# Kernel optimization log

Hardware: AMD Instinct MI355X
Metric: run time of the kernel (lower is better)

## Reference

```python
import jax, jax.numpy as jnp
import numpy as np

N_NODES = 50000
N_EDGES = 800000
VOCAB = 100000
EMB = 64
HID = 64
N_CLASSES = 10
N_GRAPHS = 512


def setup_inputs() -> dict:
    key = jax.random.key(0)
    ks = jax.random.split(key, 12)
    node_ids = jax.random.randint(ks[0], (N_NODES,), 0, VOCAB)
    edge_index = jax.random.randint(ks[1], (2, N_EDGES), 0, N_NODES)
    batch = jnp.sort(jax.random.randint(ks[2], (N_NODES,), 0, N_GRAPHS))
    emb = jax.random.normal(ks[3], (VOCAB, EMB), jnp.float32)
    s_e = 1.0 / np.sqrt(EMB)
    s_h = 1.0 / np.sqrt(HID)
    Wl0 = jax.random.normal(ks[4], (EMB, HID), jnp.float32) * s_e
    bl0 = jnp.zeros((HID,), jnp.float32)
    Wr0 = jax.random.normal(ks[5], (EMB, HID), jnp.float32) * s_e
    Wl1 = jax.random.normal(ks[6], (HID, HID), jnp.float32) * s_h
    bl1 = jnp.zeros((HID,), jnp.float32)
    Wr1 = jax.random.normal(ks[7], (HID, HID), jnp.float32) * s_h
    Wout = jax.random.normal(ks[8], (HID, N_CLASSES), jnp.float32) * s_h
    bout = jnp.zeros((N_CLASSES,), jnp.float32)
    return {"node_ids": node_ids, "edge_index": edge_index, "batch": batch,
            "emb": emb, "Wl0": Wl0, "bl0": bl0, "Wr0": Wr0,
            "Wl1": Wl1, "bl1": bl1, "Wr1": Wr1, "Wout": Wout, "bout": bout}


def _sage_conv(x, src, dst, Wl, bl, Wr):
    # PyG SAGEConv (aggr='mean'): out_i = lin_l(mean_{j in N(i)} x_j) + lin_r(x_i)
    msg = x[src]                                      # [E, d] gather
    s = jax.ops.segment_sum(msg, dst, num_segments=N_NODES)
    cnt = jax.ops.segment_sum(jnp.ones((msg.shape[0], 1), x.dtype), dst,
                              num_segments=N_NODES)
    mean = jnp.where(cnt > 0, s / jnp.maximum(cnt, 1), 0)
    return mean @ Wl + bl + x @ Wr


def reference(node_ids, edge_index, batch, emb, Wl0, bl0, Wr0, Wl1, bl1, Wr1, Wout, bout):
    x = emb[node_ids]                                  # [N, EMB]
    src, dst = edge_index[0], edge_index[1]
    x = jax.nn.relu(_sage_conv(x, src, dst, Wl0, bl0, Wr0))
    x = jax.nn.relu(_sage_conv(x, src, dst, Wl1, bl1, Wr1))
    # global_mean_pool over graph ids
    s = jax.ops.segment_sum(x, batch, num_segments=N_GRAPHS)
    cnt = jax.ops.segment_sum(jnp.ones((x.shape[0], 1), x.dtype), batch,
                              num_segments=N_GRAPHS)
    pooled = jnp.where(cnt > 0, s / jnp.maximum(cnt, 1), 0)   # [G, HID]
    return pooled @ Wout + bout                        # [G, N_CLASSES]
```

## Files before the change

kernel.cpp:

```cpp
#include <hip/hip_runtime.h>
#include <hip/hip_bf16.h>

#define N_NODES 50000
#define N_EDGES 800000
#define EMB 64
#define HID 64
#define N_CLASSES 10
#define N_GRAPHS 512

#define BKT_SHIFT 6
#define BKT_NODES 64
#define NB_BKT ((N_NODES + BKT_NODES - 1) / BKT_NODES)
#define BKT_CAP 1408
#define CNT_STRIDE 16
#define EB_CHUNK 4096
#define EB_PER_THR (EB_CHUNK / 256)
#define EB_BLOCKS ((N_EDGES + EB_CHUNK - 1) / EB_CHUNK)
#define XFORM_BLOCKS ((N_NODES + 63) / 64)
#define XPAD 68
#define ZROW N_NODES
#define LCSR_SZ 1856
#define LCSR_FULL 1864

#define ACC8(vv, A)                                                            \
    do {                                                                       \
        A[0] += __uint_as_float((vv).x << 16);                                 \
        A[1] += __uint_as_float((vv).x & 0xFFFF0000u);                         \
        A[2] += __uint_as_float((vv).y << 16);                                 \
        A[3] += __uint_as_float((vv).y & 0xFFFF0000u);                         \
        A[4] += __uint_as_float((vv).z << 16);                                 \
        A[5] += __uint_as_float((vv).z & 0xFFFF0000u);                         \
        A[6] += __uint_as_float((vv).w << 16);                                 \
        A[7] += __uint_as_float((vv).w & 0xFFFF0000u);                         \
    } while (0)

__device__ __forceinline__ void build_local_csr(
    int bucket, const int* __restrict__ cnt, const int* __restrict__ ebuf,
    unsigned short* lcsr, int* nhist, int* sval, int* sexcl, int* ncur) {
    int tid = threadIdx.x;
    int bs = bucket * BKT_CAP;
    int ne = min(cnt[bucket * CNT_STRIDE], BKT_CAP);
    if (tid < BKT_NODES) { nhist[tid] = 0; ncur[tid] = 0; }
    for (int i = tid; i < LCSR_FULL; i += 256) lcsr[i] = (unsigned short)ZROW;
    __syncthreads();
    int held[6];
    int nh = 0;
    for (int i = tid; i < ne; i += 256) held[nh++] = ebuf[bs + i];
#pragma unroll
    for (int j = 0; j < 6; j++)
        if (j < nh) atomicAdd(&nhist[held[j] >> 16], 1);
    __syncthreads();
    if (tid < 64) {
        int v = nhist[tid];
        int p = (v + 7) & ~7;
        int s = p;
#pragma unroll
        for (int off = 1; off < 64; off <<= 1) {
            int u = __shfl_up(s, off, 64);
            if (tid >= off) s += u;
        }
        sval[tid] = v;
        sexcl[tid] = s - p;
    }
    __syncthreads();
#pragma unroll
    for (int j = 0; j < 6; j++)
        if (j < nh) {
            int p = held[j];
            int l = p >> 16;
            int r = atomicAdd(&ncur[l], 1);
            lcsr[sexcl[l] + r] = (unsigned short)(p & 0xFFFF);
        }
    __syncthreads();
}

__device__ __forceinline__ void agg2(
    int sA, int dA, int sB, int dB, int sl,
    const unsigned short* lcsr, const __hip_bfloat16* __restrict__ Pb,
    float oA[8], float oB[8]) {
    float a0[8], a1[8], b0[8], b1[8];
#pragma unroll
    for (int j = 0; j < 8; j++) { a0[j] = 0.f; a1[j] = 0.f; b0[j] = 0.f; b1[j] = 0.f; }
    int nA = (dA + 3) >> 2, nB = (dB + 3) >> 2;
    int n = max(nA, nB);
    int mA = max(nA - 1, 0), mB = max(nB - 1, 0);
    if (n > 0) {
        uint4 A0[4], A1[4], B0[4], B1[4];
#define LD4(D, base_)                                                          \
        {                                                                      \
            int _p = (base_);                                                  \
            D[0] = ((const uint4*)(Pb + (size_t)lcsr[_p + 0] * 64))[sl];       \
            D[1] = ((const uint4*)(Pb + (size_t)lcsr[_p + 1] * 64))[sl];       \
            D[2] = ((const uint4*)(Pb + (size_t)lcsr[_p + 2] * 64))[sl];       \
            D[3] = ((const uint4*)(Pb + (size_t)lcsr[_p + 3] * 64))[sl];       \
        }
#define AC4(S, X0, X1)                                                         \
        { ACC8(S[0], X0); ACC8(S[1], X1); ACC8(S[2], X0); ACC8(S[3], X1); }
        LD4(A0, sA); LD4(B0, sB);
        int c = 1;
        for (; c + 1 < n; c += 2) {
            LD4(A1, sA + 4 * min(c, mA)); LD4(B1, sB + 4 * min(c, mB));
            if (c - 1 < nA) AC4(A0, a0, a1);
            if (c - 1 < nB) AC4(B0, b0, b1);
            LD4(A0, sA + 4 * min(c + 1, mA)); LD4(B0, sB + 4 * min(c + 1, mB));
            if (c < nA) AC4(A1, a0, a1);
            if (c < nB) AC4(B1, b0, b1);
        }
        if (c < n) {
            LD4(A1, sA + 4 * min(c, mA)); LD4(B1, sB + 4 * min(c, mB));
            if (c - 1 < nA) AC4(A0, a0, a1);
            if (c - 1 < nB) AC4(B0, b0, b1);
            if (c < nA) AC4(A1, a0, a1);
            if (c < nB) AC4(B1, b0, b1);
        } else {
            if (c - 1 < nA) AC4(A0, a0, a1);
            if (c - 1 < nB) AC4(B0, b0, b1);
        }
#undef LD4
#undef AC4
    }
    float invA = (dA > 0) ? 1.0f / (float)dA : 0.0f;
    float invB = (dB > 0) ? 1.0f / (float)dB : 0.0f;
#pragma unroll
    for (int j = 0; j < 8; j++) {
        oA[j] = (a0[j] + a1[j]) * invA;
        oB[j] = (b0[j] + b1[j]) * invB;
    }
}

__device__ __forceinline__ void finish_row(int node, int sl,
                                           const float* __restrict__ H,
                                           float m[8], float* dst) {
    if (node < N_NODES) {
        size_t off = (size_t)node * 64 + sl * 8;
        float4 q0 = *(const float4*)&H[off];
        float4 q1 = *(const float4*)&H[off + 4];
        m[0] = fmaxf(m[0] + q0.x, 0.f);
        m[1] = fmaxf(m[1] + q0.y, 0.f);
        m[2] = fmaxf(m[2] + q0.z, 0.f);
        m[3] = fmaxf(m[3] + q0.w, 0.f);
        m[4] = fmaxf(m[4] + q1.x, 0.f);
        m[5] = fmaxf(m[5] + q1.y, 0.f);
        m[6] = fmaxf(m[6] + q1.z, 0.f);
        m[7] = fmaxf(m[7] + q1.w, 0.f);
    } else {
#pragma unroll
        for (int j = 0; j < 8; j++) m[j] = 0.f;
    }
    *(float4*)&dst[sl * 8] = make_float4(m[0], m[1], m[2], m[3]);
    *(float4*)&dst[sl * 8 + 4] = make_float4(m[4], m[5], m[6], m[7]);
}

__device__ __forceinline__ void gemm_dual_from_sX(
    int tile, int t, const float* sX,
    const float* __restrict__ Wl, const float* __restrict__ Wr,
    const float* __restrict__ bl,
    __hip_bfloat16* __restrict__ Pb, float* __restrict__ Qout) {
    int dg = t & 15, ng = t >> 4;
    float accL[4][4], accR[4][4];
#pragma unroll
    for (int i = 0; i < 4; i++)
#pragma unroll
        for (int j = 0; j < 4; j++) { accL[i][j] = 0.f; accR[i][j] = 0.f; }
#pragma unroll 4
    for (int k = 0; k < 64; k++) {
        float4 wl = ((const float4*)Wl)[k * 16 + dg];
        float4 wr = ((const float4*)Wr)[k * 16 + dg];
#pragma unroll
        for (int i = 0; i < 4; i++) {
            float xv = sX[(ng + i * 16) * XPAD + k];
            accL[i][0] = fmaf(xv, wl.x, accL[i][0]);
            accL[i][1] = fmaf(xv, wl.y, accL[i][1]);
            accL[i][2] = fmaf(xv, wl.z, accL[i][2]);
            accL[i][3] = fmaf(xv, wl.w, accL[i][3]);
            accR[i][0] = fmaf(xv, wr.x, accR[i][0]);
            accR[i][1] = fmaf(xv, wr.y, accR[i][1]);
            accR[i][2] = fmaf(xv, wr.z, accR[i][2]);
            accR[i][3] = fmaf(xv, wr.w, accR[i][3]);
        }
    }
    float4 blv = ((const float4*)bl)[dg];
#pragma unroll
    for (int i = 0; i < 4; i++) {
        int node = tile + ng + i * 16;
        if (node < N_NODES) {
            union { ushort4 u; __hip_bfloat16 h[4]; } pk;
            pk.h[0] = __float2bfloat16(accL[i][0]);
            pk.h[1] = __float2bfloat16(accL[i][1]);
            pk.h[2] = __float2bfloat16(accL[i][2]);
            pk.h[3] = __float2bfloat16(accL[i][3]);
            *(ushort4*)&Pb[(size_t)node * 64 + dg * 4] = pk.u;
            *(float4*)&Qout[(size_t)node * 64 + dg * 4] =
                make_float4(accR[i][0] + blv.x, accR[i][1] + blv.y,
                            accR[i][2] + blv.z, accR[i][3] + blv.w);
        }
    }
}

__global__ __launch_bounds__(256) void k_combo(
    const int* __restrict__ esrc, const int* __restrict__ edst,
    int* __restrict__ cnt, int* __restrict__ ebuf,
    const int* __restrict__ ids, const float* __restrict__ emb,
    const float* __restrict__ Wl, const float* __restrict__ bl,
    const float* __restrict__ Wr,
    __hip_bfloat16* __restrict__ Pb, __hip_bfloat16* __restrict__ Pb1z,
    float* __restrict__ Qout) {
    __shared__ float sX[64 * XPAD];
    int t = threadIdx.x;
    if (blockIdx.x < EB_BLOCKS) {
        if (blockIdx.x == 0 && t < 16) {
            uint4 z = make_uint4(0u, 0u, 0u, 0u);
            if (t < 8) ((uint4*)(Pb + (size_t)ZROW * 64))[t] = z;
            else       ((uint4*)(Pb1z + (size_t)ZROW * 64))[t - 8] = z;
        }
        int* h = (int*)sX;
        int* bbase = h + NB_BKT;
        int* cur = bbase + NB_BKT;
        for (int i = t; i < NB_BKT; i += 256) { h[i] = 0; cur[i] = 0; }
        __syncthreads();
        int base = blockIdx.x * EB_CHUNK;
        int end = min(base + EB_CHUNK, N_EDGES);
        int dreg[EB_PER_THR];
        int nd = 0;
        for (int i = base + t; i < end; i += 256) dreg[nd++] = edst[i];
#pragma unroll
        for (int j = 0; j < EB_PER_THR; j++)
            if (j < nd) atomicAdd(&h[dreg[j] >> BKT_SHIFT], 1);
        __syncthreads();
        for (int i = t; i < NB_BKT; i += 256)
            if (h[i]) bbase[i] = i * BKT_CAP + atomicAdd(&cnt[i * CNT_STRIDE], h[i]);
        __syncthreads();
        {
            int j = 0;
            for (int i = base + t; i < end; i += 256, j++) {
                int d = dreg[j], s = esrc[i];
                int b = d >> BKT_SHIFT;
                int r = atomicAdd(&cur[b], 1);
                int slot = bbase[b] + r;
                if (slot < (b + 1) * BKT_CAP)
                    ebuf[slot] = ((d & (BKT_NODES - 1)) << 16) | s;
            }
        }
        return;
    }
    int tile = (blockIdx.x - EB_BLOCKS) * 64;
    for (int i = t; i < 64 * 16; i += 256) {
        int r = i >> 4, c = i & 15;
        int node = tile + r;
        float4 v = make_float4(0.f, 0.f, 0.f, 0.f);
        if (node < N_NODES)
            v = ((const float4*)(emb + (size_t)ids[node] * 64))[c];
        *(float4*)&sX[r * XPAD + c * 4] = v;
    }
    __syncthreads();
    gemm_dual_from_sX(tile, t, sX, Wl, Wr, bl, Pb, Qout);
}

__global__ __launch_bounds__(256, 4) void k_fused1(
    const int* __restrict__ cnt, const int* __restrict__ ebuf,
    const __hip_bfloat16* __restrict__ Pb0, const float* __restrict__ Wl,
    const float* __restrict__ bl, const float* __restrict__ Wr,
    __hip_bfloat16* __restrict__ Pb1, float* __restrict__ H) {
    __shared__ float sX[64 * XPAD];
    __shared__ unsigned short lcsr[LCSR_FULL];
    __shared__ int nhist[BKT_NODES], sval[BKT_NODES], sexcl[BKT_NODES], ncur[BKT_NODES];
    int t = threadIdx.x;
    int tile = blockIdx.x * 64;
    build_local_csr(blockIdx.x, cnt, ebuf, lcsr, nhist, sval, sexcl, ncur);
    int grp = t >> 3, sl = t & 7;
    int ln0 = grp * 2, ln1 = ln0 + 1;
    float mA[8], mB[8];
    agg2(sexcl[ln0], sval[ln0], sexcl[ln1], sval[ln1], sl, lcsr, Pb0, mA, mB);
    finish_row(tile + ln0, sl, H, mA, &sX[ln0 * XPAD]);
    finish_row(tile + ln1, sl, H, mB, &sX[ln1 * XPAD]);
    __syncthreads();
    gemm_dual_from_sX(tile, t, sX, Wl, Wr, bl, Pb1, H);
}

__global__ __launch_bounds__(256, 4) void k_agg2_pool(
    const int* __restrict__ cnt, const int* __restrict__ ebuf,
    const __hip_bfloat16* __restrict__ Pb, const float* __restrict__ H,
    const int* __restrict__ batch, float* __restrict__ psum) {
    __shared__ float sPool[64 * 64];
    __shared__ unsigned short lcsr[LCSR_FULL];
    __shared__ int nhist[BKT_NODES], sval[BKT_NODES], sexcl[BKT_NODES], ncur[BKT_NODES];
    __shared__ int sLg[64];
    int t = threadIdx.x;
    int nb = blockIdx.x * 64;
    int gmin = batch[nb];
    if (t < 64) {
        int node = nb + t;
        sLg[t] = batch[node < N_NODES ? node : (N_NODES - 1)] - gmin;
    }
    build_local_csr(blockIdx.x, cnt, ebuf, lcsr, nhist, sval, sexcl, ncur);
    int grp = t >> 3, sl = t & 7;
    int ln0 = grp * 2, ln1 = ln0 + 1;
    float mA[8], mB[8];
    agg2(sexcl[ln0], sval[ln0], sexcl[ln1], sval[ln1], sl, lcsr, Pb, mA, mB);
    finish_row(nb + ln0, sl, H, mA, &sPool[ln0 * 64]);
    finish_row(nb + ln1, sl, H, mB, &sPool[ln1 * 64]);
    __syncthreads();
    int d = t & 63, q = t >> 6;
    int n0 = q * 16;
    float run = 0.f;
    int cur = sLg[n0];
    for (int n = n0; n < n0 + 16; n++) {
        int lg = sLg[n];
        if (lg != cur) {
            if (run != 0.f)
                atomicAdd(&psum[(size_t)(gmin + cur) * 64 + d], run);
            run = 0.f;
            cur = lg;
        }
        run += sPool[n * 64 + d];
    }
    if (run != 0.f)
        atomicAdd(&psum[(size_t)(gmin + cur) * 64 + d], run);
}

__device__ __forceinline__ int lower_bound_batch(const int* __restrict__ batch, int val) {
    int lo = 0, hi = N_NODES;
    while (lo < hi) {
        int mid = (lo + hi) >> 1;
        if (batch[mid] < val) lo = mid + 1; else hi = mid;
    }
    return lo;
}

__global__ __launch_bounds__(256) void k_out(
    const int* __restrict__ batch, const float* __restrict__ psum,
    const float* __restrict__ Wout, const float* __restrict__ bout,
    float* __restrict__ out) {
    int w = threadIdx.x >> 6, lane = threadIdx.x & 63;
    int g = blockIdx.x * 4 + w;
    if (g >= N_GRAPHS) return;
    int s0 = lower_bound_batch(batch, g);
    int s1 = lower_bound_batch(batch, g + 1);
    int cntg = s1 - s0;
    float inv = (cntg > 0) ? 1.0f / (float)cntg : 0.0f;
    float pooled = psum[(size_t)g * 64 + lane] * inv;
#pragma unroll
    for (int c = 0; c < N_CLASSES; c++) {
        float v = pooled * Wout[lane * N_CLASSES + c];
#pragma unroll
        for (int off = 32; off > 0; off >>= 1) v += __shfl_down(v, off, 64);
        if (lane == 0) out[(size_t)g * N_CLASSES + c] = v + bout[c];
    }
}


extern "C" void kernel_launch(void* const* d_in, const int* in_sizes, int n_in,
                              void* d_out, int out_size, void* d_ws, size_t ws_size,
                              hipStream_t stream) {
    const int*   node_ids = (const int*)d_in[0];
    const int*   edge_idx = (const int*)d_in[1];
    const int*   batch    = (const int*)d_in[2];
    const float* emb      = (const float*)d_in[3];
    const float* Wl0      = (const float*)d_in[4];
    const float* bl0      = (const float*)d_in[5];
    const float* Wr0      = (const float*)d_in[6];
    const float* Wl1      = (const float*)d_in[7];
    const float* bl1      = (const float*)d_in[8];
    const float* Wr1      = (const float*)d_in[9];
    const float* Wout     = (const float*)d_in[10];
    const float* bout     = (const float*)d_in[11];
    float* out = (float*)d_out;

    const int* esrc = edge_idx;
    const int* edst = edge_idx + N_EDGES;

    __hip_bfloat16* Pb0 = (__hip_bfloat16*)d_ws;
    __hip_bfloat16* Pb1 = Pb0 + (size_t)(N_NODES + 1) * 64;
    float* H = (float*)(Pb1 + (size_t)(N_NODES + 1) * 64);
    int* ebuf = (int*)(H + (size_t)N_NODES * 64);
    int* cnt = ebuf + (size_t)NB_BKT * BKT_CAP;
    float* psum = (float*)(cnt + (size_t)NB_BKT * CNT_STRIDE);

    const int BLK = 256;

    hipMemsetAsync(cnt, 0, (NB_BKT * CNT_STRIDE + N_GRAPHS * 64) * sizeof(int), stream);

    k_combo<<<EB_BLOCKS + XFORM_BLOCKS, BLK, 0, stream>>>(
        esrc, edst, cnt, ebuf, node_ids, emb, Wl0, bl0, Wr0, Pb0, Pb1, H);

    k_fused1<<<XFORM_BLOCKS, BLK, 0, stream>>>(cnt, ebuf, Pb0, Wl1, bl1, Wr1, Pb1, H);

    k_agg2_pool<<<NB_BKT, BLK, 0, stream>>>(cnt, ebuf, Pb1, H, batch, psum);

    k_out<<<(N_GRAPHS + 3) / 4, BLK, 0, stream>>>(batch, psum, Wout, bout, out);
}
```

Measured before the change: 183.7 us.

## Split bf16 projected features into separate low and high half arrays

Stores the projected neighbor features as two separate bf16 arrays, one for the low 32 columns and one for the high 32, instead of a single 64-wide row. Aggregation now makes two passes, one per half, and each pass gathers 64-byte row segments eight neighbors at a time. The aim is a smaller gather working set per pass, so it fits better in L2/MALL and improves cache hit rates for random neighbor reads. The cost is walking the local CSR twice and issuing more, narrower (8-byte per lane) loads.

Measured after the change: 203.9 us. 11.0% more time.

```diff
diff --git a/kernel.cpp b/kernel.cpp
--- a/kernel.cpp
+++ b/kernel.cpp
@@ -22,16 +22,12 @@
 #define LCSR_SZ 1856
 #define LCSR_FULL 1864
 
-#define ACC8(vv, A)                                                            \
+#define ACC4(vv, A)                                                            \
     do {                                                                       \
         A[0] += __uint_as_float((vv).x << 16);                                 \
         A[1] += __uint_as_float((vv).x & 0xFFFF0000u);                         \
         A[2] += __uint_as_float((vv).y << 16);                                 \
         A[3] += __uint_as_float((vv).y & 0xFFFF0000u);                         \
-        A[4] += __uint_as_float((vv).z << 16);                                 \
-        A[5] += __uint_as_float((vv).z & 0xFFFF0000u);                         \
-        A[6] += __uint_as_float((vv).w << 16);                                 \
-        A[7] += __uint_as_float((vv).w & 0xFFFF0000u);                         \
     } while (0)
 
 __device__ __forceinline__ void build_local_csr(
@@ -74,88 +70,108 @@
     __syncthreads();
 }
 
-__device__ __forceinline__ void agg2(
+__device__ __forceinline__ void agg2_half(
     int sA, int dA, int sB, int dB, int sl,
-    const unsigned short* lcsr, const __hip_bfloat16* __restrict__ Pb,
-    float oA[8], float oB[8]) {
-    float a0[8], a1[8], b0[8], b1[8];
-#pragma unroll
-    for (int j = 0; j < 8; j++) { a0[j] = 0.f; a1[j] = 0.f; b0[j] = 0.f; b1[j] = 0.f; }
-    int nA = (dA + 3) >> 2, nB = (dB + 3) >> 2;
+    const unsigned short* lcsr, const __hip_bfloat16* __restrict__ P,
+    float a0[4], float a1[4], float b0[4], float b1[4]) {
+    int nA = (dA + 7) >> 3, nB = (dB + 7) >> 3;
     int n = max(nA, nB);
+    if (n <= 0) return;
     int mA = max(nA - 1, 0), mB = max(nB - 1, 0);
-    if (n > 0) {
-        uint4 A0[4], A1[4], B0[4], B1[4];
-#define LD4(D, base_)                                                          \
-        {                                                                      \
-            int _p = (base_);                                                  \
-            D[0] = ((const uint4*)(Pb + (size_t)lcsr[_p + 0] * 64))[sl];       \
-            D[1] = ((const uint4*)(Pb + (size_t)lcsr[_p + 1] * 64))[sl];       \
-            D[2] = ((const uint4*)(Pb + (size_t)lcsr[_p + 2] * 64))[sl];       \
-            D[3] = ((const uint4*)(Pb + (size_t)lcsr[_p + 3] * 64))[sl];       \
-        }
-#define AC4(S, X0, X1)                                                         \
-        { ACC8(S[0], X0); ACC8(S[1], X1); ACC8(S[2], X0); ACC8(S[3], X1); }
-        LD4(A0, sA); LD4(B0, sB);
-        int c = 1;
-        for (; c + 1 < n; c += 2) {
-            LD4(A1, sA + 4 * min(c, mA)); LD4(B1, sB + 4 * min(c, mB));
-            if (c - 1 < nA) AC4(A0, a0, a1);
-            if (c - 1 < nB) AC4(B0, b0, b1);
-            LD4(A0, sA + 4 * min(c + 1, mA)); LD4(B0, sB + 4 * min(c + 1, mB));
-            if (c < nA) AC4(A1, a0, a1);
-            if (c < nB) AC4(B1, b0, b1);
-        }
-        if (c < n) {
-            LD4(A1, sA + 4 * min(c, mA)); LD4(B1, sB + 4 * min(c, mB));
-            if (c - 1 < nA) AC4(A0, a0, a1);
-            if (c - 1 < nB) AC4(B0, b0, b1);
-            if (c < nA) AC4(A1, a0, a1);
-            if (c < nB) AC4(B1, b0, b1);
-        } else {
-            if (c - 1 < nA) AC4(A0, a0, a1);
-            if (c - 1 < nB) AC4(B0, b0, b1);
-        }
-#undef LD4
-#undef AC4
-    }
-    float invA = (dA > 0) ? 1.0f / (float)dA : 0.0f;
-    float invB = (dB > 0) ? 1.0f / (float)dB : 0.0f;
-#pragma unroll
-    for (int j = 0; j < 8; j++) {
-        oA[j] = (a0[j] + a1[j]) * invA;
-        oB[j] = (b0[j] + b1[j]) * invB;
-    }
-}
-
-__device__ __forceinline__ void finish_row(int node, int sl,
-                                           const float* __restrict__ H,
-                                           float m[8], float* dst) {
+    uint2 A0[8], A1[8], B0[8], B1[8];
+#define LD8(D, base_)                                                          \
+    {                                                                          \
+        int _p = (base_);                                                      \
+        D[0] = ((const uint2*)(P + (size_t)lcsr[_p + 0] * 32))[sl];            \
+        D[1] = ((const uint2*)(P + (size_t)lcsr[_p + 1] * 32))[sl];            \
+        D[2] = ((const uint2*)(P + (size_t)lcsr[_p + 2] * 32))[sl];            \
+        D[3] = ((const uint2*)(P + (size_t)lcsr[_p + 3] * 32))[sl];            \
+        D[4] = ((const uint2*)(P + (size_t)lcsr[_p + 4] * 32))[sl];            \
+        D[5] = ((const uint2*)(P + (size_t)lcsr[_p + 5] * 32))[sl];            \
+        D[6] = ((const uint2*)(P + (size_t)lcsr[_p + 6] * 32))[sl];            \
+        D[7] = ((const uint2*)(P + (size_t)lcsr[_p + 7] * 32))[sl];            \
+    }
+#define AC8H(S, X0, X1)                                                        \
+    { ACC4(S[0], X0); ACC4(S[1], X1); ACC4(S[2], X0); ACC4(S[3], X1);          \
+      ACC4(S[4], X0); ACC4(S[5], X1); ACC4(S[6], X0); ACC4(S[7], X1); }
+    LD8(A0, sA); LD8(B0, sB);
+    int c = 1;
+    for (; c + 1 < n; c += 2) {
+        LD8(A1, sA + 8 * min(c, mA)); LD8(B1, sB + 8 * min(c, mB));
+        if (c - 1 < nA) AC8H(A0, a0, a1);
+        if (c - 1 < nB) AC8H(B0, b0, b1);
+        LD8(A0, sA + 8 * min(c + 1, mA)); LD8(B0, sB + 8 * min(c + 1, mB));
+        if (c < nA) AC8H(A1, a0, a1);
+        if (c < nB) AC8H(B1, b0, b1);
+    }
+    if (c < n) {
+        LD8(A1, sA + 8 * min(c, mA)); LD8(B1, sB + 8 * min(c, mB));
+        if (c - 1 < nA) AC8H(A0, a0, a1);
+        if (c - 1 < nB) AC8H(B0, b0, b1);
+        if (c < nA) AC8H(A1, a0, a1);
+        if (c < nB) AC8H(B1, b0, b1);
+    } else {
+        if (c - 1 < nA) AC8H(A0, a0, a1);
+        if (c - 1 < nB) AC8H(B0, b0, b1);
+    }
+#undef LD8
+#undef AC8H
+}
+
+__device__ __forceinline__ void agg_pair_split(
+    int s0, int d0, int s1, int d1, int sl, const unsigned short* lcsr,
+    const __hip_bfloat16* __restrict__ Plo, const __hip_bfloat16* __restrict__ Phi,
+    float loA[4], float hiA[4], float loB[4], float hiB[4]) {
+    float invA = (d0 > 0) ? 1.0f / (float)d0 : 0.0f;
+    float invB = (d1 > 0) ? 1.0f / (float)d1 : 0.0f;
+    float a0[4], a1[4], b0[4], b1[4];
+#pragma unroll
+    for (int j = 0; j < 4; j++) { a0[j] = 0.f; a1[j] = 0.f; b0[j] = 0.f; b1[j] = 0.f; }
+    agg2_half(s0, d0, s1, d1, sl, lcsr, Plo, a0, a1, b0, b1);
+#pragma unroll
+    for (int j = 0; j < 4; j++) {
+        loA[j] = (a0[j] + a1[j]) * invA;
+        loB[j] = (b0[j] + b1[j]) * invB;
+        a0[j] = 0.f; a1[j] = 0.f; b0[j] = 0.f; b1[j] = 0.f;
+    }
+    agg2_half(s0, d0, s1, d1, sl, lcsr, Phi, a0, a1, b0, b1);
+#pragma unroll
+    for (int j = 0; j < 4; j++) {
+        hiA[j] = (a0[j] + a1[j]) * invA;
+        hiB[j] = (b0[j] + b1[j]) * invB;
+    }
+}
+
+__device__ __forceinline__ void finish_row2(int node, int sl,
+                                            const float* __restrict__ H,
+                                            float lo[4], float hi[4],
+                                            float* dstrow) {
     if (node < N_NODES) {
-        size_t off = (size_t)node * 64 + sl * 8;
-        float4 q0 = *(const float4*)&H[off];
-        float4 q1 = *(const float4*)&H[off + 4];
-        m[0] = fmaxf(m[0] + q0.x, 0.f);
-        m[1] = fmaxf(m[1] + q0.y, 0.f);
-        m[2] = fmaxf(m[2] + q0.z, 0.f);
-        m[3] = fmaxf(m[3] + q0.w, 0.f);
-        m[4] = fmaxf(m[4] + q1.x, 0.f);
-        m[5] = fmaxf(m[5] + q1.y, 0.f);
-        m[6] = fmaxf(m[6] + q1.z, 0.f);
-        m[7] = fmaxf(m[7] + q1.w, 0.f);
+        size_t off = (size_t)node * 64;
+        float4 q0 = *(const float4*)&H[off + sl * 4];
+        float4 q1 = *(const float4*)&H[off + 32 + sl * 4];
+        lo[0] = fmaxf(lo[0] + q0.x, 0.f);
+        lo[1] = fmaxf(lo[1] + q0.y, 0.f);
+        lo[2] = fmaxf(lo[2] + q0.z, 0.f);
+        lo[3] = fmaxf(lo[3] + q0.w, 0.f);
+        hi[0] = fmaxf(hi[0] + q1.x, 0.f);
+        hi[1] = fmaxf(hi[1] + q1.y, 0.f);
+        hi[2] = fmaxf(hi[2] + q1.z, 0.f);
+        hi[3] = fmaxf(hi[3] + q1.w, 0.f);
     } else {
 #pragma unroll
-        for (int j = 0; j < 8; j++) m[j] = 0.f;
-    }
-    *(float4*)&dst[sl * 8] = make_float4(m[0], m[1], m[2], m[3]);
-    *(float4*)&dst[sl * 8 + 4] = make_float4(m[4], m[5], m[6], m[7]);
+        for (int j = 0; j < 4; j++) { lo[j] = 0.f; hi[j] = 0.f; }
+    }
+    *(float4*)&dstrow[sl * 4] = make_float4(lo[0], lo[1], lo[2], lo[3]);
+    *(float4*)&dstrow[32 + sl * 4] = make_float4(hi[0], hi[1], hi[2], hi[3]);
 }
 
 __device__ __forceinline__ void gemm_dual_from_sX(
     int tile, int t, const float* sX,
     const float* __restrict__ Wl, const float* __restrict__ Wr,
     const float* __restrict__ bl,
-    __hip_bfloat16* __restrict__ Pb, float* __restrict__ Qout) {
+    __hip_bfloat16* __restrict__ Pb_lo, __hip_bfloat16* __restrict__ Pb_hi,
+    float* __restrict__ Qout) {
     int dg = t & 15, ng = t >> 4;
     float accL[4][4], accR[4][4];
 #pragma unroll
@@ -180,6 +196,8 @@
         }
     }
     float4 blv = ((const float4*)bl)[dg];
+    __hip_bfloat16* PbH = (dg < 8) ? Pb_lo : Pb_hi;
+    int col = (dg & 7) * 4;
 #pragma unroll
     for (int i = 0; i < 4; i++) {
         int node = tile + ng + i * 16;
@@ -189,7 +207,7 @@
             pk.h[1] = __float2bfloat16(accL[i][1]);
             pk.h[2] = __float2bfloat16(accL[i][2]);
             pk.h[3] = __float2bfloat16(accL[i][3]);
-            *(ushort4*)&Pb[(size_t)node * 64 + dg * 4] = pk.u;
+            *(ushort4*)&PbH[(size_t)node * 32 + col] = pk.u;
             *(float4*)&Qout[(size_t)node * 64 + dg * 4] =
                 make_float4(accR[i][0] + blv.x, accR[i][1] + blv.y,
                             accR[i][2] + blv.z, accR[i][3] + blv.w);
@@ -203,15 +221,18 @@
     const int* __restrict__ ids, const float* __restrict__ emb,
     const float* __restrict__ Wl, const float* __restrict__ bl,
     const float* __restrict__ Wr,
-    __hip_bfloat16* __restrict__ Pb, __hip_bfloat16* __restrict__ Pb1z,
+    __hip_bfloat16* __restrict__ P0l, __hip_bfloat16* __restrict__ P0h,
+    __hip_bfloat16* __restrict__ P1l, __hip_bfloat16* __restrict__ P1h,
     float* __restrict__ Qout) {
     __shared__ float sX[64 * XPAD];
     int t = threadIdx.x;
     if (blockIdx.x < EB_BLOCKS) {
         if (blockIdx.x == 0 && t < 16) {
             uint4 z = make_uint4(0u, 0u, 0u, 0u);
-            if (t < 8) ((uint4*)(Pb + (size_t)ZROW * 64))[t] = z;
-            else       ((uint4*)(Pb1z + (size_t)ZROW * 64))[t - 8] = z;
+            if (t < 4)       ((uint4*)(P0l + (size_t)ZROW * 32))[t] = z;
+            else if (t < 8)  ((uint4*)(P0h + (size_t)ZROW * 32))[t - 4] = z;
+            else if (t < 12) ((uint4*)(P1l + (size_t)ZROW * 32))[t - 8] = z;
+            else             ((uint4*)(P1h + (size_t)ZROW * 32))[t - 12] = z;
         }
         int* h = (int*)sX;
         int* bbase = h + NB_BKT;
@@ -253,14 +274,16 @@
         *(float4*)&sX[r * XPAD + c * 4] = v;
     }
     __syncthreads();
-    gemm_dual_from_sX(tile, t, sX, Wl, Wr, bl, Pb, Qout);
+    gemm_dual_from_sX(tile, t, sX, Wl, Wr, bl, P0l, P0h, Qout);
 }
 
 __global__ __launch_bounds__(256, 4) void k_fused1(
     const int* __restrict__ cnt, const int* __restrict__ ebuf,
-    const __hip_bfloat16* __restrict__ Pb0, const float* __restrict__ Wl,
-    const float* __restrict__ bl, const float* __restrict__ Wr,
-    __hip_bfloat16* __restrict__ Pb1, float* __restrict__ H) {
+    const __hip_bfloat16* __restrict__ P0l, const __hip_bfloat16* __restrict__ P0h,
+    const float* __restrict__ Wl, const float* __restrict__ bl,
+    const float* __restrict__ Wr,
+    __hip_bfloat16* __restrict__ P1l, __hip_bfloat16* __restrict__ P1h,
+    float* __restrict__ H) {
     __shared__ float sX[64 * XPAD];
     __shared__ unsigned short lcsr[LCSR_FULL];
     __shared__ int nhist[BKT_NODES], sval[BKT_NODES], sexcl[BKT_NODES], ncur[BKT_NODES];
@@ -269,17 +292,19 @@
     build_local_csr(blockIdx.x, cnt, ebuf, lcsr, nhist, sval, sexcl, ncur);
     int grp = t >> 3, sl = t & 7;
     int ln0 = grp * 2, ln1 = ln0 + 1;
-    float mA[8], mB[8];
-    agg2(sexcl[ln0], sval[ln0], sexcl[ln1], sval[ln1], sl, lcsr, Pb0, mA, mB);
-    finish_row(tile + ln0, sl, H, mA, &sX[ln0 * XPAD]);
-    finish_row(tile + ln1, sl, H, mB, &sX[ln1 * XPAD]);
-    __syncthreads();
-    gemm_dual_from_sX(tile, t, sX, Wl, Wr, bl, Pb1, H);
+    float loA[4], hiA[4], loB[4], hiB[4];
+    agg_pair_split(sexcl[ln0], sval[ln0], sexcl[ln1], sval[ln1], sl, lcsr,
+                   P0l, P0h, loA, hiA, loB, hiB);
+    finish_row2(tile + ln0, sl, H, loA, hiA, &sX[ln0 * XPAD]);
+    finish_row2(tile + ln1, sl, H, loB, hiB, &sX[ln1 * XPAD]);
+    __syncthreads();
+    gemm_dual_from_sX(tile, t, sX, Wl, Wr, bl, P1l, P1h, H);
 }
 
 __global__ __launch_bounds__(256, 4) void k_agg2_pool(
     const int* __restrict__ cnt, const int* __restrict__ ebuf,
-    const __hip_bfloat16* __restrict__ Pb, const float* __restrict__ H,
+    const __hip_bfloat16* __restrict__ P1l, const __hip_bfloat16* __restrict__ P1h,
+    const float* __restrict__ H,
     const int* __restrict__ batch, float* __restrict__ psum) {
     __shared__ float sPool[64 * 64];
     __shared__ unsigned short lcsr[LCSR_FULL];
@@ -295,10 +320,11 @@
     build_local_csr(blockIdx.x, cnt, ebuf, lcsr, nhist, sval, sexcl, ncur);
     int grp = t >> 3, sl = t & 7;
     int ln0 = grp * 2, ln1 = ln0 + 1;
-    float mA[8], mB[8];
-    agg2(sexcl[ln0], sval[ln0], sexcl[ln1], sval[ln1], sl, lcsr, Pb, mA, mB);
-    finish_row(nb + ln0, sl, H, mA, &sPool[ln0 * 64]);
-    finish_row(nb + ln1, sl, H, mB, &sPool[ln1 * 64]);
+    float loA[4], hiA[4], loB[4], hiB[4];
+    agg_pair_split(sexcl[ln0], sval[ln0], sexcl[ln1], sval[ln1], sl, lcsr,
+                   P1l, P1h, loA, hiA, loB, hiB);
+    finish_row2(nb + ln0, sl, H, loA, hiA, &sPool[ln0 * 64]);
+    finish_row2(nb + ln1, sl, H, loB, hiB, &sPool[ln1 * 64]);
     __syncthreads();
     int d = t & 63, q = t >> 6;
     int n0 = q * 16;
@@ -369,9 +395,11 @@
     const int* esrc = edge_idx;
     const int* edst = edge_idx + N_EDGES;
 
-    __hip_bfloat16* Pb0 = (__hip_bfloat16*)d_ws;
-    __hip_bfloat16* Pb1 = Pb0 + (size_t)(N_NODES + 1) * 64;
-    float* H = (float*)(Pb1 + (size_t)(N_NODES + 1) * 64);
+    __hip_bfloat16* P0l = (__hip_bfloat16*)d_ws;
+    __hip_bfloat16* P0h = P0l + (size_t)(N_NODES + 1) * 32;
+    __hip_bfloat16* P1l = P0h + (size_t)(N_NODES + 1) * 32;
+    __hip_bfloat16* P1h = P1l + (size_t)(N_NODES + 1) * 32;
+    float* H = (float*)(P1h + (size_t)(N_NODES + 1) * 32);
     int* ebuf = (int*)(H + (size_t)N_NODES * 64);
     int* cnt = ebuf + (size_t)NB_BKT * BKT_CAP;
     float* psum = (float*)(cnt + (size_t)NB_BKT * CNT_STRIDE);
@@ -381,11 +409,13 @@
     hipMemsetAsync(cnt, 0, (NB_BKT * CNT_STRIDE + N_GRAPHS * 64) * sizeof(int), stream);
 
     k_combo<<<EB_BLOCKS + XFORM_BLOCKS, BLK, 0, stream>>>(
-        esrc, edst, cnt, ebuf, node_ids, emb, Wl0, bl0, Wr0, Pb0, Pb1, H);
-
-    k_fused1<<<XFORM_BLOCKS, BLK, 0, stream>>>(cnt, ebuf, Pb0, Wl1, bl1, Wr1, Pb1, H);
-
-    k_agg2_pool<<<NB_BKT, BLK, 0, stream>>>(cnt, ebuf, Pb1, H, batch, psum);
+        esrc, edst, cnt, ebuf, node_ids, emb, Wl0, bl0, Wr0,
+        P0l, P0h, P1l, P1h, H);
+
+    k_fused1<<<XFORM_BLOCKS, BLK, 0, stream>>>(cnt, ebuf, P0l, P0h,
+                                               Wl1, bl1, Wr1, P1l, P1h, H);
+
+    k_agg2_pool<<<NB_BKT, BLK, 0, stream>>>(cnt, ebuf, P1l, P1h, H, batch, psum);
 
     k_out<<<(N_GRAPHS + 3) / 4, BLK, 0, stream>>>(batch, psum, Wout, bout, out);
 }
```

## Double block size to 512 threads, one node per 8-lane group in aggregation

Applied to the files above, without the earlier changes.

Blocks grow from 256 to 512 threads in all main kernels. Each 8-lane group now aggregates one destination node instead of two interleaved ones, loading eight neighbours per step. The per-thread GEMM tile, edge-binning and CSR-build loops shrink to match. This gives more parallelism and fewer registers per thread. The cost is less memory-level parallelism per thread and heavier block-level barriers.

Result: slower. 233.4 us (+27.1%).

```diff
diff --git a/kernel.cpp b/kernel.cpp
--- a/kernel.cpp
+++ b/kernel.cpp
@@ -14,7 +14,7 @@
 #define BKT_CAP 1408
 #define CNT_STRIDE 16
 #define EB_CHUNK 4096
-#define EB_PER_THR (EB_CHUNK / 256)
+#define EB_PER_THR (EB_CHUNK / 512)
 #define EB_BLOCKS ((N_EDGES + EB_CHUNK - 1) / EB_CHUNK)
 #define XFORM_BLOCKS ((N_NODES + 63) / 64)
 #define XPAD 68
@@ -41,13 +41,13 @@
     int bs = bucket * BKT_CAP;
     int ne = min(cnt[bucket * CNT_STRIDE], BKT_CAP);
     if (tid < BKT_NODES) { nhist[tid] = 0; ncur[tid] = 0; }
-    for (int i = tid; i < LCSR_FULL; i += 256) lcsr[i] = (unsigned short)ZROW;
-    __syncthreads();
-    int held[6];
+    for (int i = tid; i < LCSR_FULL; i += 512) lcsr[i] = (unsigned short)ZROW;
+    __syncthreads();
+    int held[3];
     int nh = 0;
-    for (int i = tid; i < ne; i += 256) held[nh++] = ebuf[bs + i];
-#pragma unroll
-    for (int j = 0; j < 6; j++)
+    for (int i = tid; i < ne; i += 512) held[nh++] = ebuf[bs + i];
+#pragma unroll
+    for (int j = 0; j < 3; j++)
         if (j < nh) atomicAdd(&nhist[held[j] >> 16], 1);
     __syncthreads();
     if (tid < 64) {
@@ -64,7 +64,7 @@
     }
     __syncthreads();
 #pragma unroll
-    for (int j = 0; j < 6; j++)
+    for (int j = 0; j < 3; j++)
         if (j < nh) {
             int p = held[j];
             int l = p >> 16;
@@ -74,58 +74,52 @@
     __syncthreads();
 }
 
-__device__ __forceinline__ void agg2(
-    int sA, int dA, int sB, int dB, int sl,
+__device__ __forceinline__ void agg1(
+    int s0, int deg, int sl,
     const unsigned short* lcsr, const __hip_bfloat16* __restrict__ Pb,
-    float oA[8], float oB[8]) {
-    float a0[8], a1[8], b0[8], b1[8];
-#pragma unroll
-    for (int j = 0; j < 8; j++) { a0[j] = 0.f; a1[j] = 0.f; b0[j] = 0.f; b1[j] = 0.f; }
-    int nA = (dA + 3) >> 2, nB = (dB + 3) >> 2;
-    int n = max(nA, nB);
-    int mA = max(nA - 1, 0), mB = max(nB - 1, 0);
+    float out[8]) {
+    float a0[8], a1[8];
+#pragma unroll
+    for (int j = 0; j < 8; j++) { a0[j] = 0.f; a1[j] = 0.f; }
+    int n = (deg + 7) >> 3;
     if (n > 0) {
-        uint4 A0[4], A1[4], B0[4], B1[4];
-#define LD4(D, base_)                                                          \
+        uint4 A0[8], A1[8];
+#define LD8(D, base_)                                                          \
         {                                                                      \
             int _p = (base_);                                                  \
             D[0] = ((const uint4*)(Pb + (size_t)lcsr[_p + 0] * 64))[sl];       \
             D[1] = ((const uint4*)(Pb + (size_t)lcsr[_p + 1] * 64))[sl];       \
             D[2] = ((const uint4*)(Pb + (size_t)lcsr[_p + 2] * 64))[sl];       \
             D[3] = ((const uint4*)(Pb + (size_t)lcsr[_p + 3] * 64))[sl];       \
-        }
-#define AC4(S, X0, X1)                                                         \
-        { ACC8(S[0], X0); ACC8(S[1], X1); ACC8(S[2], X0); ACC8(S[3], X1); }
-        LD4(A0, sA); LD4(B0, sB);
+            D[4] = ((const uint4*)(Pb + (size_t)lcsr[_p + 4] * 64))[sl];       \
+            D[5] = ((const uint4*)(Pb + (size_t)lcsr[_p + 5] * 64))[sl];       \
+            D[6] = ((const uint4*)(Pb + (size_t)lcsr[_p + 6] * 64))[sl];       \
+            D[7] = ((const uint4*)(Pb + (size_t)lcsr[_p + 7] * 64))[sl];       \
+        }
+#define AC8(S)                                                                 \
+        { ACC8(S[0], a0); ACC8(S[1], a1); ACC8(S[2], a0); ACC8(S[3], a1);      \
+          ACC8(S[4], a0); ACC8(S[5], a1); ACC8(S[6], a0); ACC8(S[7], a1); }
+        LD8(A0, s0);
         int c = 1;
         for (; c + 1 < n; c += 2) {
-            LD4(A1, sA + 4 * min(c, mA)); LD4(B1, sB + 4 * min(c, mB));
-            if (c - 1 < nA) AC4(A0, a0, a1);
-            if (c - 1 < nB) AC4(B0, b0, b1);
-            LD4(A0, sA + 4 * min(c + 1, mA)); LD4(B0, sB + 4 * min(c + 1, mB));
-            if (c < nA) AC4(A1, a0, a1);
-            if (c < nB) AC4(B1, b0, b1);
+            LD8(A1, s0 + 8 * c);
+            AC8(A0);
+            LD8(A0, s0 + 8 * (c + 1));
+            AC8(A1);
         }
         if (c < n) {
-            LD4(A1, sA + 4 * min(c, mA)); LD4(B1, sB + 4 * min(c, mB));
-            if (c - 1 < nA) AC4(A0, a0, a1);
-            if (c - 1 < nB) AC4(B0, b0, b1);
-            if (c < nA) AC4(A1, a0, a1);
-            if (c < nB) AC4(B1, b0, b1);
+            LD8(A1, s0 + 8 * c);
+            AC8(A0);
+            AC8(A1);
         } else {
-            if (c - 1 < nA) AC4(A0, a0, a1);
-            if (c - 1 < nB) AC4(B0, b0, b1);
-        }
-#undef LD4
-#undef AC4
-    }
-    float invA = (dA > 0) ? 1.0f / (float)dA : 0.0f;
-    float invB = (dB > 0) ? 1.0f / (float)dB : 0.0f;
-#pragma unroll
-    for (int j = 0; j < 8; j++) {
-        oA[j] = (a0[j] + a1[j]) * invA;
-        oB[j] = (b0[j] + b1[j]) * invB;
-    }
+            AC8(A0);
+        }
+#undef LD8
+#undef AC8
+    }
+    float inv = (deg > 0) ? 1.0f / (float)deg : 0.0f;
+#pragma unroll
+    for (int j = 0; j < 8; j++) out[j] = (a0[j] + a1[j]) * inv;
 }
 
 __device__ __forceinline__ void finish_row(int node, int sl,
@@ -157,9 +151,9 @@
     const float* __restrict__ bl,
     __hip_bfloat16* __restrict__ Pb, float* __restrict__ Qout) {
     int dg = t & 15, ng = t >> 4;
-    float accL[4][4], accR[4][4];
-#pragma unroll
-    for (int i = 0; i < 4; i++)
+    float accL[2][4], accR[2][4];
+#pragma unroll
+    for (int i = 0; i < 2; i++)
 #pragma unroll
         for (int j = 0; j < 4; j++) { accL[i][j] = 0.f; accR[i][j] = 0.f; }
 #pragma unroll 4
@@ -167,8 +161,8 @@
         float4 wl = ((const float4*)Wl)[k * 16 + dg];
         float4 wr = ((const float4*)Wr)[k * 16 + dg];
 #pragma unroll
-        for (int i = 0; i < 4; i++) {
-            float xv = sX[(ng + i * 16) * XPAD + k];
+        for (int i = 0; i < 2; i++) {
+            float xv = sX[(ng + i * 32) * XPAD + k];
             accL[i][0] = fmaf(xv, wl.x, accL[i][0]);
             accL[i][1] = fmaf(xv, wl.y, accL[i][1]);
             accL[i][2] = fmaf(xv, wl.z, accL[i][2]);
@@ -181,8 +175,8 @@
     }
     float4 blv = ((const float4*)bl)[dg];
 #pragma unroll
-    for (int i = 0; i < 4; i++) {
-        int node = tile + ng + i * 16;
+    for (int i = 0; i < 2; i++) {
+        int node = tile + ng + i * 32;
         if (node < N_NODES) {
             union { ushort4 u; __hip_bfloat16 h[4]; } pk;
             pk.h[0] = __float2bfloat16(accL[i][0]);
@@ -197,7 +191,7 @@
     }
 }
 
-__global__ __launch_bounds__(256) void k_combo(
+__global__ __launch_bounds__(512, 4) void k_combo(
     const int* __restrict__ esrc, const int* __restrict__ edst,
     int* __restrict__ cnt, int* __restrict__ ebuf,
     const int* __restrict__ ids, const float* __restrict__ emb,
@@ -216,23 +210,23 @@
         int* h = (int*)sX;
         int* bbase = h + NB_BKT;
         int* cur = bbase + NB_BKT;
-        for (int i = t; i < NB_BKT; i += 256) { h[i] = 0; cur[i] = 0; }
+        for (int i = t; i < NB_BKT; i += 512) { h[i] = 0; cur[i] = 0; }
         __syncthreads();
         int base = blockIdx.x * EB_CHUNK;
         int end = min(base + EB_CHUNK, N_EDGES);
         int dreg[EB_PER_THR];
         int nd = 0;
-        for (int i = base + t; i < end; i += 256) dreg[nd++] = edst[i];
+        for (int i = base + t; i < end; i += 512) dreg[nd++] = edst[i];
 #pragma unroll
         for (int j = 0; j < EB_PER_THR; j++)
             if (j < nd) atomicAdd(&h[dreg[j] >> BKT_SHIFT], 1);
         __syncthreads();
-        for (int i = t; i < NB_BKT; i += 256)
+        for (int i = t; i < NB_BKT; i += 512)
             if (h[i]) bbase[i] = i * BKT_CAP + atomicAdd(&cnt[i * CNT_STRIDE], h[i]);
         __syncthreads();
         {
             int j = 0;
-            for (int i = base + t; i < end; i += 256, j++) {
+            for (int i = base + t; i < end; i += 512, j++) {
                 int d = dreg[j], s = esrc[i];
                 int b = d >> BKT_SHIFT;
                 int r = atomicAdd(&cur[b], 1);
@@ -244,7 +238,7 @@
         return;
     }
     int tile = (blockIdx.x - EB_BLOCKS) * 64;
-    for (int i = t; i < 64 * 16; i += 256) {
+    for (int i = t; i < 64 * 16; i += 512) {
         int r = i >> 4, c = i & 15;
         int node = tile + r;
         float4 v = make_float4(0.f, 0.f, 0.f, 0.f);
@@ -256,7 +250,7 @@
     gemm_dual_from_sX(tile, t, sX, Wl, Wr, bl, Pb, Qout);
 }
 
-__global__ __launch_bounds__(256, 4) void k_fused1(
+__global__ __launch_bounds__(512, 4) void k_fused1(
     const int* __restrict__ cnt, const int* __restrict__ ebuf,
     const __hip_bfloat16* __restrict__ Pb0, const float* __restrict__ Wl,
     const float* __restrict__ bl, const float* __restrict__ Wr,
@@ -268,16 +262,14 @@
     int tile = blockIdx.x * 64;
     build_local_csr(blockIdx.x, cnt, ebuf, lcsr, nhist, sval, sexcl, ncur);
     int grp = t >> 3, sl = t & 7;
-    int ln0 = grp * 2, ln1 = ln0 + 1;
-    float mA[8], mB[8];
-    agg2(sexcl[ln0], sval[ln0], sexcl[ln1], sval[ln1], sl, lcsr, Pb0, mA, mB);
-    finish_row(tile + ln0, sl, H, mA, &sX[ln0 * XPAD]);
-    finish_row(tile + ln1, sl, H, mB, &sX[ln1 * XPAD]);
+    float m[8];
+    agg1(sexcl[grp], sval[grp], sl, lcsr, Pb0, m);
+    finish_row(tile + grp, sl, H, m, &sX[grp * XPAD]);
     __syncthreads();
     gemm_dual_from_sX(tile, t, sX, Wl, Wr, bl, Pb1, H);
 }
 
-__global__ __launch_bounds__(256, 4) void k_agg2_pool(
+__global__ __launch_bounds__(512, 4) void k_agg2_pool(
     const int* __restrict__ cnt, const int* __restrict__ ebuf,
     const __hip_bfloat16* __restrict__ Pb, const float* __restrict__ H,
     const int* __restrict__ batch, float* __restrict__ psum) {
@@ -294,17 +286,15 @@
     }
     build_local_csr(blockIdx.x, cnt, ebuf, lcsr, nhist, sval, sexcl, ncur);
     int grp = t >> 3, sl = t & 7;
-    int ln0 = grp * 2, ln1 = ln0 + 1;
-    float mA[8], mB[8];
-    agg2(sexcl[ln0], sval[ln0], sexcl[ln1], sval[ln1], sl, lcsr, Pb, mA, mB);
-    finish_row(nb + ln0, sl, H, mA, &sPool[ln0 * 64]);
-    finish_row(nb + ln1, sl, H, mB, &sPool[ln1 * 64]);
+    float m[8];
+    agg1(sexcl[grp], sval[grp], sl, lcsr, Pb, m);
+    finish_row(nb + grp, sl, H, m, &sPool[grp * 64]);
     __syncthreads();
     int d = t & 63, q = t >> 6;
-    int n0 = q * 16;
+    int n0 = q * 8;
     float run = 0.f;
     int cur = sLg[n0];
-    for (int n = n0; n < n0 + 16; n++) {
+    for (int n = n0; n < n0 + 8; n++) {
         int lg = sLg[n];
         if (lg != cur) {
             if (run != 0.f)
@@ -376,16 +366,17 @@
     int* cnt = ebuf + (size_t)NB_BKT * BKT_CAP;
     float* psum = (float*)(cnt + (size_t)NB_BKT * CNT_STRIDE);
 
-    const int BLK = 256;
+    const int BLK = 512;
 
     hipMemsetAsync(cnt, 0, (NB_BKT * CNT_STRIDE + N_GRAPHS * 64) * sizeof(int), stream);
 
     k_combo<<<EB_BLOCKS + XFORM_BLOCKS, BLK, 0, stream>>>(
         esrc, edst, cnt, ebuf, node_ids, emb, Wl0, bl0, Wr0, Pb0, Pb1, H);
 
-    k_fused1<<<XFORM_BLOCKS, BLK, 0, stream>>>(cnt, ebuf, Pb0, Wl1, bl1, Wr1, Pb1, H);
+    k_fused1<<<XFORM_BLOCKS, BLK, 0, stream>>>(cnt, ebuf, Pb0, Wl1, bl1, Wr1,
+                                               Pb1, H);
 
     k_agg2_pool<<<NB_BKT, BLK, 0, stream>>>(cnt, ebuf, Pb1, H, batch, psum);
 
-    k_out<<<(N_GRAPHS + 3) / 4, BLK, 0, stream>>>(batch, psum, Wout, bout, out);
-}
+    k_out<<<(N_GRAPHS + 3) / 4, 256, 0, stream>>>(batch, psum, Wout, bout, out);
+}
```
